# Performance work log

Hardware: AMD Instinct MI355X
Metric: run time of the kernel (lower is better)

The kernel has to match this reference:

```python
import jax, jax.numpy as jnp
import numpy as np

HID = 10  # hidden_dim


def conv1x1(x, w, b=None):
    # x: [N,C,H,W], w: [O,C] -> [N,O,H,W]
    y = jnp.einsum('oc,nchw->nohw', w, x)
    if b is not None:
        y = y + b[None, :, None, None]
    return y


def gconv1x1(x, w, b=None):
    # grouped 1x1 conv. x: [N,G*ipg,H,W], w: [G,opg,ipg]
    N, C, H, W = x.shape
    G, opg, ipg = w.shape
    xg = x.reshape(N, G, ipg, H, W)
    y = jnp.einsum('goi,ngihw->ngohw', w, xg).reshape(N, G * opg, H, W)
    if b is not None:
        y = y + b[None, :, None, None]
    return y


def _decomp(h_fea, xf, xh, att_w, att_b, w):
    # Decomposition: spatial attention from (fea, xf, xh), gate xf, project.
    att = jax.nn.sigmoid(conv1x1(jnp.concatenate([h_fea, xf, xh], axis=1), att_w, att_b))
    xfh = jax.nn.relu(conv1x1(xf * att, w))
    return xfh, att


def _comp(parts, xh, att_w, att_b, w):
    # Composition: parts [P,N,HID,H,W]; grouped per-part attention then fuse with xh.
    ca = jax.nn.sigmoid(jnp.einsum('pc,pnchw->pnhw', att_w[:, 0], parts) + att_b[:, None, None, None])
    msg = (parts * ca[:, :, None]).sum(0)  # [N,HID,H,W]
    return jax.nn.relu(conv1x1(jnp.concatenate([xh, msg], axis=1), w))


def _update(xh, m0, m1, m2, gate_w, gate_b, cand_w):
    # conv_Update: gated residual update from summed messages.
    cat = jnp.concatenate([xh, m0 + m1 + m2], axis=1)
    g = jax.nn.sigmoid(conv1x1(cat, gate_w, gate_b))
    cand = jax.nn.relu(conv1x1(cat, cand_w))
    return xh * (1.0 - g) + cand * g


def half_graph(h_fea, xh_u, xh_l, xf, xp, pdp_w1, pdp_w2, att_w, att_b,
               compU_att_w, compU_att_b, compU_w,
               compL_att_w, compL_att_b, compL_w,
               decU_att_w, decU_att_b, decU_w,
               decL_att_w, decL_att_b, decL_w,
               updU_gate_w, updU_gate_b, updU_cand_w,
               updL_gate_w, updL_gate_b, updL_cand_w):
    # Part_Dependency: shared trunk then grouped conv -> (dp_u, dp_l)
    t = jax.nn.relu(conv1x1(jnp.concatenate([h_fea, xh_u, xh_l], axis=1), pdp_w1))
    dp = jax.nn.relu(gconv1x1(t, pdp_w2))
    dp_u, dp_l = dp[:, :HID], dp[:, HID:]
    # grouped sigmoid attention over the two half nodes
    a = jax.nn.sigmoid(gconv1x1(jnp.concatenate([xh_u, xh_l], axis=1), att_w, att_b))
    ag_u, ag_l = a[:, 0:1], a[:, 1:2]
    # upper half node
    xphu = _comp(xp[0:4], xh_u, compU_att_w, compU_att_b, compU_w)
    xlh = dp_l * ag_l + xh_u * ag_u  # Pair_Part_Dependency (lower -> upper)
    xfhu, att_u = _decomp(h_fea, xf, xh_u, decU_att_w, decU_att_b, decU_w)
    xh_u_new = _update(xh_u, xphu, xlh, xfhu, updU_gate_w, updU_gate_b, updU_cand_w)
    # lower half node
    xphl = _comp(xp[4:6], xh_l, compL_att_w, compL_att_b, compL_w)
    xuh = dp_u * ag_u + xh_l * ag_l  # Pair_Part_Dependency (upper -> lower)
    xfhl, att_l = _decomp(h_fea, xf, xh_l, decL_att_w, decL_att_b, decL_w)
    xh_l_new = _update(xh_l, xphl, xuh, xfhl, updL_gate_w, updL_gate_b, updL_cand_w)
    return xh_u_new, xh_l_new, att_u, att_l


def setup_inputs() -> dict:
    key = jax.random.key(0)
    N, C, H, W = 8, 256, 128, 128
    ks = jax.random.split(key, 32)
    s = 0.05
    inp = {
        'h_fea': jax.random.normal(ks[0], (N, C, H, W), jnp.float32),
        'xh_u': jax.random.normal(ks[1], (N, HID, H, W), jnp.float32),
        'xh_l': jax.random.normal(ks[2], (N, HID, H, W), jnp.float32),
        'xf': jax.random.normal(ks[3], (N, HID, H, W), jnp.float32),
        'xp': jax.random.normal(ks[4], (6, N, HID, H, W), jnp.float32),
        'pdp_w1': jax.random.normal(ks[5], (2 * HID, C + 2 * HID), jnp.float32) * s,
        'pdp_w2': jax.random.normal(ks[6], (2, HID, HID), jnp.float32) * s,
        'att_w': jax.random.normal(ks[7], (2, 1, HID), jnp.float32) * s,
        'att_b': jnp.zeros((2,), jnp.float32),
        'compU_att_w': jax.random.normal(ks[8], (4, 1, HID), jnp.float32) * s,
        'compU_att_b': jnp.zeros((4,), jnp.float32),
        'compU_w': jax.random.normal(ks[9], (HID, 2 * HID), jnp.float32) * s,
        'compL_att_w': jax.random.normal(ks[10], (2, 1, HID), jnp.float32) * s,
        'compL_att_b': jnp.zeros((2,), jnp.float32),
        'compL_w': jax.random.normal(ks[11], (HID, 2 * HID), jnp.float32) * s,
        'decU_att_w': jax.random.normal(ks[12], (1, C + 2 * HID), jnp.float32) * s,
        'decU_att_b': jnp.zeros((1,), jnp.float32),
        'decU_w': jax.random.normal(ks[13], (HID, HID), jnp.float32) * s,
        'decL_att_w': jax.random.normal(ks[14], (1, C + 2 * HID), jnp.float32) * s,
        'decL_att_b': jnp.zeros((1,), jnp.float32),
        'decL_w': jax.random.normal(ks[15], (HID, HID), jnp.float32) * s,
        'updU_gate_w': jax.random.normal(ks[16], (HID, 2 * HID), jnp.float32) * s,
        'updU_gate_b': jnp.zeros((HID,), jnp.float32),
        'updU_cand_w': jax.random.normal(ks[17], (HID, 2 * HID), jnp.float32) * s,
        'updL_gate_w': jax.random.normal(ks[18], (HID, 2 * HID), jnp.float32) * s,
        'updL_gate_b': jnp.zeros((HID,), jnp.float32),
        'updL_cand_w': jax.random.normal(ks[19], (HID, 2 * HID), jnp.float32) * s,
    }
    return inp


def reference(h_fea, xh_u, xh_l, xf, xp, pdp_w1, pdp_w2, att_w, att_b,
              compU_att_w, compU_att_b, compU_w,
              compL_att_w, compL_att_b, compL_w,
              decU_att_w, decU_att_b, decU_w,
              decL_att_w, decL_att_b, decL_w,
              updU_gate_w, updU_gate_b, updU_cand_w,
              updL_gate_w, updL_gate_b, updL_cand_w):
    return half_graph(h_fea, xh_u, xh_l, xf, xp, pdp_w1, pdp_w2, att_w, att_b,
                      compU_att_w, compU_att_b, compU_w,
                      compL_att_w, compL_att_b, compL_w,
                      decU_att_w, decU_att_b, decU_w,
                      decL_att_w, decL_att_b, decL_w,
                      updU_gate_w, updU_gate_b, updU_cand_w,
                      updL_gate_w, updL_gate_b, updL_cand_w)
```

## Files before the change

kernel.cpp:

```cpp
#include <hip/hip_runtime.h>
#include <stdint.h>

typedef unsigned short u16;
typedef unsigned int   u32;

#define HW   16384
#define NPIX 131072

__device__ __forceinline__ float sigm(float x) { return 1.f / (1.f + __expf(-x)); }

__global__ __launch_bounds__(256) void half_graph_fused(
    const float* __restrict__ hf,  const float* __restrict__ xhu, const float* __restrict__ xhl,
    const float* __restrict__ xfg, const float* __restrict__ xpg,
    const float* __restrict__ pdp_w1, const float* __restrict__ pdp_w2,
    const float* __restrict__ att_w,  const float* __restrict__ att_b,
    const float* __restrict__ cU_aw, const float* __restrict__ cU_ab, const float* __restrict__ cU_w,
    const float* __restrict__ cL_aw, const float* __restrict__ cL_ab, const float* __restrict__ cL_w,
    const float* __restrict__ dU_aw, const float* __restrict__ dU_ab, const float* __restrict__ dU_w,
    const float* __restrict__ dL_aw, const float* __restrict__ dL_ab, const float* __restrict__ dL_w,
    const float* __restrict__ uU_gw, const float* __restrict__ uU_gb, const float* __restrict__ uU_cw,
    const float* __restrict__ uL_gw, const float* __restrict__ uL_gb, const float* __restrict__ uL_cw,
    float* __restrict__ out)
{
    __shared__ float lds[256 * 24];

    const int tid = threadIdx.x;
    const int wv  = tid >> 6;
    const int ln  = tid & 63;
    const int p   = blockIdx.x * 64 + ln;
    const int n   = p >> 14;
    const int hw  = p & 16383;

    for (int idx = tid; idx < 22 * 256; idx += 256) {
        int o = idx >> 8, c = idx & 255;
        float w = (o < 20) ? pdp_w1[o * 276 + c]
                           : (o == 20 ? dU_aw[c] : dL_aw[c]);
        lds[c * 24 + o] = w;
    }
    __syncthreads();

    const float* hfp = hf + ((size_t)n * 256 + wv * 64) * HW + hw;
    float acc[22];
    #pragma unroll
    for (int o = 0; o < 22; ++o) acc[o] = 0.f;

    #pragma unroll 8
    for (int cc = 0; cc < 64; ++cc) {
        float x = hfp[cc * HW];
        const float* wr = &lds[(wv * 64 + cc) * 24];
        #pragma unroll
        for (int o = 0; o < 22; ++o) acc[o] = fmaf(wr[o], x, acc[o]);
    }
    __syncthreads();

    #pragma unroll
    for (int o = 0; o < 22; ++o) lds[o * 256 + wv * 64 + ln] = acc[o];
    __syncthreads();

    if (wv != 0) return;

    float accT[22];
    #pragma unroll
    for (int o = 0; o < 22; ++o)
        accT[o] = (lds[o * 256 + ln]       + lds[o * 256 + 64 + ln])
                + (lds[o * 256 + 128 + ln] + lds[o * 256 + 192 + ln]);
    const float dU = accT[20], dL = accT[21];

    float xu[10], xl[10], xv[10];
    {
        const float* a = xhu + (size_t)n * 10 * HW + hw;
        const float* b = xhl + (size_t)n * 10 * HW + hw;
        const float* c = xfg + (size_t)n * 10 * HW + hw;
        #pragma unroll
        for (int i = 0; i < 10; ++i) xu[i] = a[i * HW];
        #pragma unroll
        for (int i = 0; i < 10; ++i) xl[i] = b[i * HW];
        #pragma unroll
        for (int i = 0; i < 10; ++i) xv[i] = c[i * HW];
    }

    float t[20];
    #pragma unroll
    for (int o = 0; o < 20; ++o) {
        float s = accT[o];
        #pragma unroll
        for (int i = 0; i < 10; ++i) s = fmaf(pdp_w1[o * 276 + 256 + i], xu[i], s);
        #pragma unroll
        for (int i = 0; i < 10; ++i) s = fmaf(pdp_w1[o * 276 + 266 + i], xl[i], s);
        t[o] = fmaxf(s, 0.f);
    }
    float dpv[20];
    #pragma unroll
    for (int g = 0; g < 2; ++g) {
        #pragma unroll
        for (int o = 0; o < 10; ++o) {
            float s = 0.f;
            #pragma unroll
            for (int i = 0; i < 10; ++i)
                s = fmaf(pdp_w2[(g * 10 + o) * 10 + i], t[g * 10 + i], s);
            dpv[g * 10 + o] = fmaxf(s, 0.f);
        }
    }

    float au_s = att_b[0], al_s = att_b[1];
    #pragma unroll
    for (int i = 0; i < 10; ++i) {
        au_s = fmaf(att_w[i], xu[i], au_s);
        al_s = fmaf(att_w[10 + i], xl[i], al_s);
    }
    const float au = sigm(au_s), al = sigm(al_s);

    float su = dU + dU_ab[0];
    float sl = dL + dL_ab[0];
    #pragma unroll
    for (int i = 0; i < 10; ++i) { su = fmaf(dU_aw[256 + i], xv[i], su); sl = fmaf(dL_aw[256 + i], xv[i], sl); }
    #pragma unroll
    for (int i = 0; i < 10; ++i) { su = fmaf(dU_aw[266 + i], xu[i], su); sl = fmaf(dL_aw[266 + i], xl[i], sl); }
    const float attU = sigm(su), attL = sigm(sl);

    float xfhu[10], xfhl[10];
    #pragma unroll
    for (int o = 0; o < 10; ++o) {
        float a = 0.f, b = 0.f;
        #pragma unroll
        for (int i = 0; i < 10; ++i) {
            a = fmaf(dU_w[o * 10 + i], xv[i], a);
            b = fmaf(dL_w[o * 10 + i], xv[i], b);
        }
        xfhu[o] = fmaxf(attU * a, 0.f);
        xfhl[o] = fmaxf(attL * b, 0.f);
    }

    float msgU[10];
    #pragma unroll
    for (int i = 0; i < 10; ++i) msgU[i] = 0.f;
    #pragma unroll
    for (int pp = 0; pp < 4; ++pp) {
        const float* xq = xpg + (size_t)(pp * 8 + n) * 10 * HW + hw;
        float v[10];
        #pragma unroll
        for (int i = 0; i < 10; ++i) v[i] = xq[i * HW];
        float s = cU_ab[pp];
        #pragma unroll
        for (int i = 0; i < 10; ++i) s = fmaf(cU_aw[pp * 10 + i], v[i], s);
        float ca = sigm(s);
        #pragma unroll
        for (int i = 0; i < 10; ++i) msgU[i] = fmaf(ca, v[i], msgU[i]);
    }
    float xphu[10];
    #pragma unroll
    for (int o = 0; o < 10; ++o) {
        float s = 0.f;
        #pragma unroll
        for (int i = 0; i < 10; ++i) s = fmaf(cU_w[o * 20 + i], xu[i], s);
        #pragma unroll
        for (int i = 0; i < 10; ++i) s = fmaf(cU_w[o * 20 + 10 + i], msgU[i], s);
        xphu[o] = fmaxf(s, 0.f);
    }

    float msgL[10];
    #pragma unroll
    for (int i = 0; i < 10; ++i) msgL[i] = 0.f;
    #pragma unroll
    for (int pp = 4; pp < 6; ++pp) {
        const float* xq = xpg + (size_t)(pp * 8 + n) * 10 * HW + hw;
        float v[10];
        #pragma unroll
        for (int i = 0; i < 10; ++i) v[i] = xq[i * HW];
        float s = cL_ab[pp - 4];
        #pragma unroll
        for (int i = 0; i < 10; ++i) s = fmaf(cL_aw[(pp - 4) * 10 + i], v[i], s);
        float ca = sigm(s);
        #pragma unroll
        for (int i = 0; i < 10; ++i) msgL[i] = fmaf(ca, v[i], msgL[i]);
    }
    float xphl[10];
    #pragma unroll
    for (int o = 0; o < 10; ++o) {
        float s = 0.f;
        #pragma unroll
        for (int i = 0; i < 10; ++i) s = fmaf(cL_w[o * 20 + i], xl[i], s);
        #pragma unroll
        for (int i = 0; i < 10; ++i) s = fmaf(cL_w[o * 20 + 10 + i], msgL[i], s);
        xphl[o] = fmaxf(s, 0.f);
    }

    float outU[10], outL[10];
    {
        float m[10];
        #pragma unroll
        for (int i = 0; i < 10; ++i)
            m[i] = xphu[i] + (dpv[10 + i] * al + xu[i] * au) + xfhu[i];
        #pragma unroll
        for (int o = 0; o < 10; ++o) {
            float gs = uU_gb[o], cs = 0.f;
            #pragma unroll
            for (int i = 0; i < 10; ++i) {
                gs = fmaf(uU_gw[o * 20 + i], xu[i], gs);
                cs = fmaf(uU_cw[o * 20 + i], xu[i], cs);
            }
            #pragma unroll
            for (int i = 0; i < 10; ++i) {
                gs = fmaf(uU_gw[o * 20 + 10 + i], m[i], gs);
                cs = fmaf(uU_cw[o * 20 + 10 + i], m[i], cs);
            }
            float g = sigm(gs), cd = fmaxf(cs, 0.f);
            outU[o] = xu[o] * (1.f - g) + cd * g;
        }
    }
    {
        float m[10];
        #pragma unroll
        for (int i = 0; i < 10; ++i)
            m[i] = xphl[i] + (dpv[i] * au + xl[i] * al) + xfhl[i];
        #pragma unroll
        for (int o = 0; o < 10; ++o) {
            float gs = uL_gb[o], cs = 0.f;
            #pragma unroll
            for (int i = 0; i < 10; ++i) {
                gs = fmaf(uL_gw[o * 20 + i], xl[i], gs);
                cs = fmaf(uL_cw[o * 20 + i], xl[i], cs);
            }
            #pragma unroll
            for (int i = 0; i < 10; ++i) {
                gs = fmaf(uL_gw[o * 20 + 10 + i], m[i], gs);
                cs = fmaf(uL_cw[o * 20 + 10 + i], m[i], cs);
            }
            float g = sigm(gs), cd = fmaxf(cs, 0.f);
            outL[o] = xl[o] * (1.f - g) + cd * g;
        }
    }

    {
        int baseU = n * 10 * HW + hw;
        #pragma unroll
        for (int c = 0; c < 10; ++c) out[baseU + c * HW] = outU[c];
        int baseL = 1310720 + baseU;
        #pragma unroll
        for (int c = 0; c < 10; ++c) out[baseL + c * HW] = outL[c];
        out[2621440 + n * HW + hw] = attU;
        out[2752512 + n * HW + hw] = attL;
    }
}

extern "C" void kernel_launch(void* const* d_in, const int* in_sizes, int n_in,
                              void* d_out, int out_size, void* d_ws, size_t ws_size,
                              hipStream_t stream) {
    (void)in_sizes; (void)n_in; (void)out_size; (void)d_ws; (void)ws_size;
    const float* hf   = (const float*)d_in[0];
    const float* xhu  = (const float*)d_in[1];
    const float* xhl  = (const float*)d_in[2];
    const float* xfg  = (const float*)d_in[3];
    const float* xpg  = (const float*)d_in[4];
    const float* w1   = (const float*)d_in[5];
    const float* w2   = (const float*)d_in[6];
    const float* aw   = (const float*)d_in[7];
    const float* ab   = (const float*)d_in[8];
    const float* cUaw = (const float*)d_in[9];
    const float* cUab = (const float*)d_in[10];
    const float* cUw  = (const float*)d_in[11];
    const float* cLaw = (const float*)d_in[12];
    const float* cLab = (const float*)d_in[13];
    const float* cLw  = (const float*)d_in[14];
    const float* dUaw = (const float*)d_in[15];
    const float* dUab = (const float*)d_in[16];
    const float* dUw  = (const float*)d_in[17];
    const float* dLaw = (const float*)d_in[18];
    const float* dLab = (const float*)d_in[19];
    const float* dLw  = (const float*)d_in[20];
    const float* uUgw = (const float*)d_in[21];
    const float* uUgb = (const float*)d_in[22];
    const float* uUcw = (const float*)d_in[23];
    const float* uLgw = (const float*)d_in[24];
    const float* uLgb = (const float*)d_in[25];
    const float* uLcw = (const float*)d_in[26];

    dim3 grid(NPIX / 64), block(256);
    hipLaunchKernelGGL(half_graph_fused, grid, block, 0, stream,
        hf, xhu, xhl, xfg, xpg, w1, w2, aw, ab,
        cUaw, cUab, cUw, cLaw, cLab, cLw,
        dUaw, dUab, dUw, dLaw, dLab, dLw,
        uUgw, uUgb, uUcw, uLgw, uLgb, uLcw,
        (float*)d_out);
}
```

Before: 304.0 us.

## Keep pdp weights in registers and broadcast via readlane instead of LDS

Each lane now loads one channel's 22 weights into registers, and the inner loop broadcasts them with readlane rather than reading them from LDS. This removes the cooperative LDS weight staging and one barrier. The reduction buffer shrinks to a padded [4][22][66] array, and launch bounds request six blocks per CU to raise occupancy. The risk is that readlane with a loop-unrolled lane index generates SGPR moves that could serialize the FMA stream, and the occupancy hint may force register spills.

```diff
diff --git a/kernel.cpp b/kernel.cpp
--- a/kernel.cpp
+++ b/kernel.cpp
@@ -8,8 +8,11 @@
 #define NPIX 131072
 
 __device__ __forceinline__ float sigm(float x) { return 1.f / (1.f + __expf(-x)); }
-
-__global__ __launch_bounds__(256) void half_graph_fused(
+__device__ __forceinline__ float rdlane(float v, int lane) {
+    return __int_as_float(__builtin_amdgcn_readlane(__float_as_int(v), lane));
+}
+
+__global__ __launch_bounds__(256, 6) void half_graph_fused(
     const float* __restrict__ hf,  const float* __restrict__ xhu, const float* __restrict__ xhl,
     const float* __restrict__ xfg, const float* __restrict__ xpg,
     const float* __restrict__ pdp_w1, const float* __restrict__ pdp_w2,
@@ -22,49 +25,45 @@
     const float* __restrict__ uL_gw, const float* __restrict__ uL_gb, const float* __restrict__ uL_cw,
     float* __restrict__ out)
 {
-    __shared__ float lds[256 * 24];
+    __shared__ float red[4][22][66];
 
     const int tid = threadIdx.x;
     const int wv  = tid >> 6;
     const int ln  = tid & 63;
-    const int p   = blockIdx.x * 64 + ln;
-    const int n   = p >> 14;
-    const int hw  = p & 16383;
-
-    for (int idx = tid; idx < 22 * 256; idx += 256) {
-        int o = idx >> 8, c = idx & 255;
-        float w = (o < 20) ? pdp_w1[o * 276 + c]
-                           : (o == 20 ? dU_aw[c] : dL_aw[c]);
-        lds[c * 24 + o] = w;
-    }
-    __syncthreads();
-
-    const float* hfp = hf + ((size_t)n * 256 + wv * 64) * HW + hw;
+    const int pb  = blockIdx.x;
+    const int n   = pb >> 8;
+    const int hw  = ((pb & 255) << 6) + ln;
+
+    float w[22];
+    #pragma unroll
+    for (int o = 0; o < 20; ++o) w[o] = pdp_w1[o * 276 + wv * 64 + ln];
+    w[20] = dU_aw[wv * 64 + ln];
+    w[21] = dL_aw[wv * 64 + ln];
+
     float acc[22];
     #pragma unroll
     for (int o = 0; o < 22; ++o) acc[o] = 0.f;
 
+    const float* xb = hf + ((size_t)n * 256 + wv * 64) * HW + hw;
     #pragma unroll 8
     for (int cc = 0; cc < 64; ++cc) {
-        float x = hfp[cc * HW];
-        const float* wr = &lds[(wv * 64 + cc) * 24];
-        #pragma unroll
-        for (int o = 0; o < 22; ++o) acc[o] = fmaf(wr[o], x, acc[o]);
-    }
+        float x = xb[(size_t)cc * HW];
+        #pragma unroll
+        for (int o = 0; o < 22; ++o)
+            acc[o] = fmaf(rdlane(w[o], cc), x, acc[o]);
+    }
+
+    #pragma unroll
+    for (int o = 0; o < 22; ++o) red[wv][o][ln] = acc[o];
     __syncthreads();
-
-    #pragma unroll
-    for (int o = 0; o < 22; ++o) lds[o * 256 + wv * 64 + ln] = acc[o];
-    __syncthreads();
-
     if (wv != 0) return;
 
-    float accT[22];
-    #pragma unroll
-    for (int o = 0; o < 22; ++o)
-        accT[o] = (lds[o * 256 + ln]       + lds[o * 256 + 64 + ln])
-                + (lds[o * 256 + 128 + ln] + lds[o * 256 + 192 + ln]);
-    const float dU = accT[20], dL = accT[21];
+    float accT[20];
+    #pragma unroll
+    for (int o = 0; o < 20; ++o)
+        accT[o] = (red[0][o][ln] + red[1][o][ln]) + (red[2][o][ln] + red[3][o][ln]);
+    const float dU = (red[0][20][ln] + red[1][20][ln]) + (red[2][20][ln] + red[3][20][ln]);
+    const float dL = (red[0][21][ln] + red[1][21][ln]) + (red[2][21][ln] + red[3][21][ln]);
 
     float xu[10], xl[10], xv[10];
     {
```

New measurement: 339.7 us. 1.12x slower.
